# Kernel tuning notes

Hardware: AMD Instinct MI355X
Metric: run time of the kernel (lower is better)

## Reference

```python
import jax, jax.numpy as jnp
import numpy as np

N, E = 10000, 320000
IN, H, C, ED = 256, 4, 64, 64
HC = H * C
EPS = 1e-5
NEG_SLOPE = 0.2


def setup_inputs() -> dict:
    key = jax.random.key(0)
    ks = jax.random.split(key, 12)
    g = lambda k, shape, fan: jax.random.normal(k, shape, jnp.float32) * (1.0 / np.sqrt(fan))
    return {
        "x": jax.random.normal(ks[0], (N, IN), jnp.float32),
        "edge_index": jax.random.randint(ks[1], (2, E), 0, N, jnp.int64),
        "edge_attr": jax.random.normal(ks[2], (E, ED), jnp.float32),
        "Wl": g(ks[3], (HC, IN), IN),   # lin_l weight (source)
        "bl": jnp.zeros((HC,), jnp.float32),
        "Wr": g(ks[4], (HC, IN), IN),   # lin_r weight (target)
        "br": jnp.zeros((HC,), jnp.float32),
        "We": g(ks[5], (HC, ED), ED),   # lin_edge weight (no bias)
        "att": g(ks[6], (H, C), C),
        "bias": jnp.zeros((HC,), jnp.float32),
        "gamma": jnp.ones((HC,), jnp.float32),
        "beta": jnp.zeros((HC,), jnp.float32),
    }


def reference(x, edge_index, edge_attr, Wl, bl, Wr, br, We, att, bias, gamma, beta):
    src, dst = edge_index[0], edge_index[1]
    # add_self_loops with fill_value='mean': loop edge_attr = mean of incoming attrs
    ones = jnp.ones((E,), jnp.float32)
    cnt = jax.ops.segment_sum(ones, dst, num_segments=N)              # [N]
    loop_attr = jax.ops.segment_sum(edge_attr, dst, num_segments=N) / jnp.maximum(cnt, 1.0)[:, None]
    node_ids = jnp.arange(N, dtype=src.dtype)
    src_f = jnp.concatenate([src, node_ids])                          # [E+N]
    dst_f = jnp.concatenate([dst, node_ids])
    ea = jnp.concatenate([edge_attr, loop_attr], axis=0)              # [E+N, ED]

    xl = (x @ Wl.T + bl).reshape(N, H, C)   # source-side projection
    xr = (x @ Wr.T + br).reshape(N, H, C)   # target-side projection
    ep = (ea @ We.T).reshape(-1, H, C)       # edge projection

    m = xl[src_f] + xr[dst_f] + ep                                    # [E+N, H, C]
    m = jnp.where(m >= 0, m, NEG_SLOPE * m)                           # leaky_relu(0.2)
    logits = jnp.einsum("ehc,hc->eh", m, att)                        # [E+N, H]

    # segment softmax over target node dst_f (every node has a self loop)
    mx = jax.ops.segment_max(logits, dst_f, num_segments=N)
    ex = jnp.exp(logits - mx[dst_f])
    den = jax.ops.segment_sum(ex, dst_f, num_segments=N)
    alpha = ex / den[dst_f]                                           # [E+N, H]

    out = jax.ops.segment_sum(xl[src_f] * alpha[:, :, None], dst_f, num_segments=N)
    h = out.reshape(N, HC) + bias

    # SiLU then LayerNorm, dropout is identity in eval
    h = h * jax.nn.sigmoid(h)
    mu = jnp.mean(h, axis=-1, keepdims=True)
    var = jnp.mean((h - mu) ** 2, axis=-1, keepdims=True)
    h = (h - mu) * jax.lax.rsqrt(var + EPS) * gamma + beta
    return h, alpha
```

## Files before the change

kernel.cpp:

```cpp
#include <hip/hip_runtime.h>

#define N_NODES 10000
#define N_EDGES 320000
#define NE_TOT  330000
#define NEG_SLOPE 0.2f
#define LN_EPS 1e-5f

#define OFF_CNT    0u
#define OFF_FILL   40000u
#define OFF_ROWPTR 80128u
#define OFF_EIDS   120320u
#define OFF_POSE   1440512u
#define OFF_XLH    4000512u
#define OFF_XRH    9120512u
#define OFF_LOG    14240512u
#define OFF_WLF    19520512u
#define OFF_WRF    19651584u
#define OFF_WEF    19782656u
#define OFF_SD     19815424u
#define OFF_EAC    21135424u

typedef __bf16 bf16x8 __attribute__((ext_vector_type(8)));
typedef float  f32x4  __attribute__((ext_vector_type(4)));
typedef unsigned short us4 __attribute__((ext_vector_type(4)));

__device__ __forceinline__ float bf2f(unsigned short u) {
    union { unsigned int i; float f; } v;
    v.i = ((unsigned int)u) << 16;
    return v.f;
}
__device__ __forceinline__ float lo2f(unsigned int u) {
    union { unsigned int i; float f; } v;
    v.i = u << 16;
    return v.f;
}
__device__ __forceinline__ float hi2f(unsigned int u) {
    union { unsigned int i; float f; } v;
    v.i = u & 0xFFFF0000u;
    return v.f;
}
__device__ __forceinline__ unsigned short f2bf(float x) {
    __bf16 b = (__bf16)x;
    return __builtin_bit_cast(unsigned short, b);
}
__device__ __forceinline__ bf16x8 cvt8(const float* p) {
    float4 v0 = *reinterpret_cast<const float4*>(p);
    float4 v1 = *reinterpret_cast<const float4*>(p + 4);
    bf16x8 t;
    t[0] = (__bf16)v0.x; t[1] = (__bf16)v0.y; t[2] = (__bf16)v0.z; t[3] = (__bf16)v0.w;
    t[4] = (__bf16)v1.x; t[5] = (__bf16)v1.y; t[6] = (__bf16)v1.z; t[7] = (__bf16)v1.w;
    return t;
}

__global__ void k_count(const int* __restrict__ ei, int* __restrict__ cnt) {
    int e = blockIdx.x * blockDim.x + threadIdx.x;
    if (e < N_EDGES) atomicAdd(&cnt[ei[N_EDGES + e]], 1);
}

__global__ void k_scan(const int* __restrict__ cnt, int* __restrict__ row_ptr) {
    __shared__ int sums[1024];
    int t = threadIdx.x;
    const int CH = 10;
    int base = t * CH;
    int s = 0;
    for (int i = 0; i < CH; i++) {
        int n = base + i;
        if (n < N_NODES) s += cnt[n] + 1;
    }
    sums[t] = s;
    __syncthreads();
    for (int off = 1; off < 1024; off <<= 1) {
        int v = (t >= off) ? sums[t - off] : 0;
        __syncthreads();
        sums[t] += v;
        __syncthreads();
    }
    int run = (t == 0) ? 0 : sums[t - 1];
    for (int i = 0; i < CH; i++) {
        int n = base + i;
        if (n < N_NODES) { row_ptr[n] = run; run += cnt[n] + 1; }
    }
    if (t == 1023) row_ptr[N_NODES] = sums[1023];
}

__global__ void k_fill(const int* __restrict__ ei, const int* __restrict__ row_ptr,
                       int* __restrict__ fill, int* __restrict__ eids,
                       int* __restrict__ sdv, int* __restrict__ pose) {
    int e = blockIdx.x * blockDim.x + threadIdx.x;
    if (e >= NE_TOT) return;
    int s, d;
    if (e < N_EDGES) { s = ei[e]; d = ei[N_EDGES + e]; }
    else             { s = e - N_EDGES; d = s; }
    int pos = atomicAdd(&fill[d], 1);
    int p = row_ptr[d] + pos;
    eids[p] = e;
    sdv[p] = s | (d << 16);
    pose[e] = p;
}

__global__ void k_permute_e(const float* __restrict__ edge_attr,
                            const int* __restrict__ pose,
                            unsigned short* __restrict__ eac) {
    int idx = blockIdx.x * blockDim.x + threadIdx.x;
    if (idx >= N_EDGES * 32) return;
    int e = idx >> 5, cp = idx & 31;
    float2 v = reinterpret_cast<const float2*>(edge_attr)[(size_t)e * 32 + cp];
    int p = pose[e];
    unsigned int u = ((unsigned int)f2bf(v.x)) | (((unsigned int)f2bf(v.y)) << 16);
    reinterpret_cast<unsigned int*>(eac)[(size_t)p * 32 + cp] = u;
}

__global__ void k_self_attr(const int* __restrict__ row_ptr,
                            const int* __restrict__ pose,
                            unsigned short* __restrict__ eac) {
    int node = (blockIdx.x << 2) + (threadIdx.x >> 6);
    int lane = threadIdx.x & 63;
    int b = row_ptr[node], en = row_ptr[node + 1];
    int selfp = pose[N_EDGES + node];
    float s0 = 0.0f, s1 = 0.0f;
    int i = b;
    for (; i + 1 < en; i += 2) {
        float a0 = bf2f(eac[(size_t)(i + 0) * 64 + lane]);
        float a1 = bf2f(eac[(size_t)(i + 1) * 64 + lane]);
        s0 += (i + 0 == selfp) ? 0.0f : a0;
        s1 += (i + 1 == selfp) ? 0.0f : a1;
    }
    for (; i < en; i++) {
        float a = bf2f(eac[(size_t)i * 64 + lane]);
        s0 += (i == selfp) ? 0.0f : a;
    }
    float s = s0 + s1;
    float c = (float)(en - b - 1);
    eac[(size_t)selfp * 64 + lane] = f2bf(s / fmaxf(c, 1.0f));
}

__global__ void k_prep_wfrag(const float* __restrict__ Wl,
                             const float* __restrict__ Wr,
                             const float* __restrict__ We,
                             unsigned short* __restrict__ wlf,
                             unsigned short* __restrict__ wrf,
                             unsigned short* __restrict__ wef) {
    int idx = blockIdx.x * 256 + threadIdx.x;
    if (idx >= 8192) return;
    int ln = idx & 63;
    int ts = (idx >> 6) & 7;
    int ct = idx >> 9;
    int c = ct * 16 + (ln & 15);
    int k0 = ts * 32 + (ln >> 4) * 8;
    *reinterpret_cast<bf16x8*>(wlf + (size_t)idx * 8) = cvt8(Wl + (size_t)c * 256 + k0);
    *reinterpret_cast<bf16x8*>(wrf + (size_t)idx * 8) = cvt8(Wr + (size_t)c * 256 + k0);
    if (idx < 2048) {
        int f = idx >> 6;
        int cb = f >> 1, step = f & 1;
        int ce = cb * 16 + (ln & 15);
        int ke = step * 32 + (ln >> 4) * 8;
        *reinterpret_cast<bf16x8*>(wef + (size_t)idx * 8) = cvt8(We + (size_t)ce * 64 + ke);
    }
}

__global__ __launch_bounds__(256) void k_gemm_mfma(
        const float* __restrict__ x,
        const float* __restrict__ bl, const float* __restrict__ br,
        const unsigned short* __restrict__ wlf,
        const unsigned short* __restrict__ wrf,
        unsigned short* __restrict__ xlh,
        unsigned short* __restrict__ xrh) {
    __shared__ __bf16 xs[8 * 64 * 8];
    int tid = threadIdx.x;
    int nb = blockIdx.x * 16;

    for (int f = tid; f < 512; f += 256) {
        int t = f >> 6, ln = f & 63;
        int node = nb + (ln & 15);
        int k0 = t * 32 + (ln >> 4) * 8;
        *reinterpret_cast<bf16x8*>(&xs[f * 8]) = cvt8(x + (size_t)node * 256 + k0);
    }
    __syncthreads();

    int lane = tid & 63;
    int wv = tid >> 6;
    int quad = lane >> 4;
    int ln15 = lane & 15;

    bf16x8 bfr[8];
#pragma unroll
    for (int t = 0; t < 8; t++)
        bfr[t] = *reinterpret_cast<const bf16x8*>(&xs[(t * 64 + lane) * 8]);

    int node = nb + ln15;
#pragma unroll
    for (int ci = 0; ci < 4; ci++) {
        int ct = wv * 4 + ci;
        f32x4 accl, accr;
        accl[0] = accl[1] = accl[2] = accl[3] = 0.0f;
        accr[0] = accr[1] = accr[2] = accr[3] = 0.0f;
#pragma unroll
        for (int t = 0; t < 8; t++) {
            bf16x8 al = *reinterpret_cast<const bf16x8*>(
                wlf + ((size_t)(ct * 8 + t) * 64 + lane) * 8);
            accl = __builtin_amdgcn_mfma_f32_16x16x32_bf16(al, bfr[t], accl, 0, 0, 0);
        }
#pragma unroll
        for (int t = 0; t < 8; t++) {
            bf16x8 ar = *reinterpret_cast<const bf16x8*>(
                wrf + ((size_t)(ct * 8 + t) * 64 + lane) * 8);
            accr = __builtin_amdgcn_mfma_f32_16x16x32_bf16(ar, bfr[t], accr, 0, 0, 0);
        }
        int cbase = ct * 16 + quad * 4;
        float4 blv = *reinterpret_cast<const float4*>(bl + cbase);
        float4 brv = *reinterpret_cast<const float4*>(br + cbase);
        us4 ol, orr;
        ol[0] = f2bf(accl[0] + blv.x); ol[1] = f2bf(accl[1] + blv.y);
        ol[2] = f2bf(accl[2] + blv.z); ol[3] = f2bf(accl[3] + blv.w);
        orr[0] = f2bf(accr[0] + brv.x); orr[1] = f2bf(accr[1] + brv.y);
        orr[2] = f2bf(accr[2] + brv.z); orr[3] = f2bf(accr[3] + brv.w);
        *reinterpret_cast<us4*>(xlh + (size_t)node * 256 + cbase) = ol;
        *reinterpret_cast<us4*>(xrh + (size_t)node * 256 + cbase) = orr;
    }
}

__global__ __launch_bounds__(256) void k_logits_mfma(
        const int* __restrict__ sdv,
        const unsigned short* __restrict__ eac,
        const unsigned short* __restrict__ xlh,
        const unsigned short* __restrict__ xrh,
        const unsigned short* __restrict__ wef,
        const float* __restrict__ att,
        float* __restrict__ logits) {
    __shared__ __bf16 wef_s[2048 * 8];
    __shared__ float att_s[256];
    int tid = threadIdx.x;

    for (int f = tid; f < 2048; f += 256) {
        *reinterpret_cast<bf16x8*>(&wef_s[(size_t)f * 8]) =
            *reinterpret_cast<const bf16x8*>(wef + (size_t)f * 8);
    }
    if (tid < 64) {
        reinterpret_cast<float4*>(att_s)[tid] =
            reinterpret_cast<const float4*>(att)[tid];
    }
    __syncthreads();

    int lane = tid & 63;
    int wv = tid >> 6;
    int quad = lane >> 4;
    int ln15 = lane & 15;

    const int ntiles = NE_TOT / 16;
#pragma unroll 1
    for (int t = blockIdx.x * 4 + wv; t < ntiles; t += gridDim.x * 4) {
        int pos = t * 16 + ln15;
        int sd = sdv[pos];
        int s = sd & 0xFFFF;
        int d = sd >> 16;
        const unsigned short* row = eac + (size_t)pos * 64;
        const uint2* xls = reinterpret_cast<const uint2*>(xlh + (size_t)s * 256);
        const uint2* xrd = reinterpret_cast<const uint2*>(xrh + (size_t)d * 256);

        bf16x8 bfr0 = *reinterpret_cast<const bf16x8*>(row + quad * 8);
        bf16x8 bfr1 = *reinterpret_cast<const bf16x8*>(row + 32 + quad * 8);
        uint2 xa[16], xb[16];
#pragma unroll
        for (int cb = 0; cb < 16; cb++) {
            int ci = cb * 4 + quad;
            xa[cb] = xls[ci];
            xb[cb] = xrd[ci];
        }
#pragma unroll
        for (int cb = 0; cb < 16; cb++) {
            asm volatile("" : "+v"(xa[cb].x), "+v"(xa[cb].y),
                              "+v"(xb[cb].x), "+v"(xb[cb].y));
        }
        __builtin_amdgcn_sched_barrier(0);

        float hsum[4] = {0.0f, 0.0f, 0.0f, 0.0f};
#pragma unroll
        for (int cb = 0; cb < 16; cb++) {
            f32x4 acc;
            acc[0] = acc[1] = acc[2] = acc[3] = 0.0f;
            bf16x8 a0 = *reinterpret_cast<const bf16x8*>(
                &wef_s[((size_t)(cb * 2 + 0) * 64 + lane) * 8]);
            bf16x8 a1 = *reinterpret_cast<const bf16x8*>(
                &wef_s[((size_t)(cb * 2 + 1) * 64 + lane) * 8]);
            acc = __builtin_amdgcn_mfma_f32_16x16x32_bf16(a0, bfr0, acc, 0, 0, 0);
            acc = __builtin_amdgcn_mfma_f32_16x16x32_bf16(a1, bfr1, acc, 0, 0, 0);

            int cbase = cb * 16 + quad * 4;
            float4 at = *reinterpret_cast<const float4*>(&att_s[cbase]);
            float x0 = lo2f(xa[cb].x) + lo2f(xb[cb].x);
            float x1 = hi2f(xa[cb].x) + hi2f(xb[cb].x);
            float x2 = lo2f(xa[cb].y) + lo2f(xb[cb].y);
            float x3 = hi2f(xa[cb].y) + hi2f(xb[cb].y);
            float v0 = acc[0] + x0; v0 = fmaxf(v0, NEG_SLOPE * v0);
            float v1 = acc[1] + x1; v1 = fmaxf(v1, NEG_SLOPE * v1);
            float v2 = acc[2] + x2; v2 = fmaxf(v2, NEG_SLOPE * v2);
            float v3 = acc[3] + x3; v3 = fmaxf(v3, NEG_SLOPE * v3);
            float hs = fmaf(v0, at.x, fmaf(v1, at.y, fmaf(v2, at.z, v3 * at.w)));
            hsum[cb >> 2] += hs;
        }
#pragma unroll
        for (int hh = 0; hh < 4; hh++) {
            hsum[hh] += __shfl_xor(hsum[hh], 16, 64);
            hsum[hh] += __shfl_xor(hsum[hh], 32, 64);
        }
        if (quad == 0) {
            reinterpret_cast<float4*>(logits)[pos] =
                make_float4(hsum[0], hsum[1], hsum[2], hsum[3]);
        }
    }
}

__global__ void k_aggregate(const int* __restrict__ sdv,
                            const int* __restrict__ row_ptr,
                            const int* __restrict__ eids,
                            const float* __restrict__ logits,
                            const unsigned short* __restrict__ xlh,
                            const float* __restrict__ bias,
                            const float* __restrict__ gamma,
                            const float* __restrict__ beta,
                            float* __restrict__ hout,
                            float* __restrict__ alpha_out) {
    int node = (blockIdx.x << 2) + (threadIdx.x >> 6);
    int lane = threadIdx.x & 63;
    int h = lane >> 4;
    int b = row_ptr[node], en = row_ptr[node + 1];
    const uint2* xl2 = reinterpret_cast<const uint2*>(xlh);

    float m0 = -INFINITY, m1 = -INFINITY, m2 = -INFINITY, m3 = -INFINITY;
    int i = b;
    for (; i + 3 < en; i += 4) {
        m0 = fmaxf(m0, logits[(i + 0) * 4 + h]);
        m1 = fmaxf(m1, logits[(i + 1) * 4 + h]);
        m2 = fmaxf(m2, logits[(i + 2) * 4 + h]);
        m3 = fmaxf(m3, logits[(i + 3) * 4 + h]);
    }
    for (; i < en; i++) m0 = fmaxf(m0, logits[i * 4 + h]);
    float mh = fmaxf(fmaxf(m0, m1), fmaxf(m2, m3));

    float d0 = 0.0f, d1 = 0.0f, d2 = 0.0f, d3 = 0.0f;
    i = b;
    for (; i + 3 < en; i += 4) {
        d0 += __expf(logits[(i + 0) * 4 + h] - mh);
        d1 += __expf(logits[(i + 1) * 4 + h] - mh);
        d2 += __expf(logits[(i + 2) * 4 + h] - mh);
        d3 += __expf(logits[(i + 3) * 4 + h] - mh);
    }
    for (; i < en; i++) d0 += __expf(logits[i * 4 + h] - mh);
    float rden = 1.0f / ((d0 + d1) + (d2 + d3));

    float4 ac0; ac0.x = ac0.y = ac0.z = ac0.w = 0.0f;
    float4 ac1; ac1.x = ac1.y = ac1.z = ac1.w = 0.0f;
    i = b;
    for (; i + 7 < en; i += 8) {
        int sd0 = sdv[i + 0], sd1 = sdv[i + 1], sd2 = sdv[i + 2], sd3 = sdv[i + 3];
        int sd4 = sdv[i + 4], sd5 = sdv[i + 5], sd6 = sdv[i + 6], sd7 = sdv[i + 7];
        float lg0 = logits[(i + 0) * 4 + h], lg1 = logits[(i + 1) * 4 + h];
        float lg2 = logits[(i + 2) * 4 + h], lg3 = logits[(i + 3) * 4 + h];
        float lg4 = logits[(i + 4) * 4 + h], lg5 = logits[(i + 5) * 4 + h];
        float lg6 = logits[(i + 6) * 4 + h], lg7 = logits[(i + 7) * 4 + h];
        int e0 = eids[i + 0], e1 = eids[i + 1], e2 = eids[i + 2], e3 = eids[i + 3];
        int e4 = eids[i + 4], e5 = eids[i + 5], e6 = eids[i + 6], e7 = eids[i + 7];
        uint2 x0 = xl2[(size_t)(sd0 & 0xFFFF) * 64 + lane];
        uint2 x1 = xl2[(size_t)(sd1 & 0xFFFF) * 64 + lane];
        uint2 x2 = xl2[(size_t)(sd2 & 0xFFFF) * 64 + lane];
        uint2 x3 = xl2[(size_t)(sd3 & 0xFFFF) * 64 + lane];
        uint2 x4 = xl2[(size_t)(sd4 & 0xFFFF) * 64 + lane];
        uint2 x5 = xl2[(size_t)(sd5 & 0xFFFF) * 64 + lane];
        uint2 x6 = xl2[(size_t)(sd6 & 0xFFFF) * 64 + lane];
        uint2 x7 = xl2[(size_t)(sd7 & 0xFFFF) * 64 + lane];
        asm volatile("" : "+v"(x0.x), "+v"(x0.y), "+v"(x1.x), "+v"(x1.y),
                          "+v"(x2.x), "+v"(x2.y), "+v"(x3.x), "+v"(x3.y));
        asm volatile("" : "+v"(x4.x), "+v"(x4.y), "+v"(x5.x), "+v"(x5.y),
                          "+v"(x6.x), "+v"(x6.y), "+v"(x7.x), "+v"(x7.y));

        float al0 = __expf(lg0 - mh) * rden;
        float al1 = __expf(lg1 - mh) * rden;
        float al2 = __expf(lg2 - mh) * rden;
        float al3 = __expf(lg3 - mh) * rden;
        float al4 = __expf(lg4 - mh) * rden;
        float al5 = __expf(lg5 - mh) * rden;
        float al6 = __expf(lg6 - mh) * rden;
        float al7 = __expf(lg7 - mh) * rden;
        if ((lane & 15) == 0) {
            alpha_out[e0 * 4 + h] = al0; alpha_out[e1 * 4 + h] = al1;
            alpha_out[e2 * 4 + h] = al2; alpha_out[e3 * 4 + h] = al3;
            alpha_out[e4 * 4 + h] = al4; alpha_out[e5 * 4 + h] = al5;
            alpha_out[e6 * 4 + h] = al6; alpha_out[e7 * 4 + h] = al7;
        }
        ac0.x = fmaf(al0, lo2f(x0.x), ac0.x); ac0.y = fmaf(al0, hi2f(x0.x), ac0.y);
        ac0.z = fmaf(al0, lo2f(x0.y), ac0.z); ac0.w = fmaf(al0, hi2f(x0.y), ac0.w);
        ac1.x = fmaf(al1, lo2f(x1.x), ac1.x); ac1.y = fmaf(al1, hi2f(x1.x), ac1.y);
        ac1.z = fmaf(al1, lo2f(x1.y), ac1.z); ac1.w = fmaf(al1, hi2f(x1.y), ac1.w);
        ac0.x = fmaf(al2, lo2f(x2.x), ac0.x); ac0.y = fmaf(al2, hi2f(x2.x), ac0.y);
        ac0.z = fmaf(al2, lo2f(x2.y), ac0.z); ac0.w = fmaf(al2, hi2f(x2.y), ac0.w);
        ac1.x = fmaf(al3, lo2f(x3.x), ac1.x); ac1.y = fmaf(al3, hi2f(x3.x), ac1.y);
        ac1.z = fmaf(al3, lo2f(x3.y), ac1.z); ac1.w = fmaf(al3, hi2f(x3.y), ac1.w);
        ac0.x = fmaf(al4, lo2f(x4.x), ac0.x); ac0.y = fmaf(al4, hi2f(x4.x), ac0.y);
        ac0.z = fmaf(al4, lo2f(x4.y), ac0.z); ac0.w = fmaf(al4, hi2f(x4.y), ac0.w);
        ac1.x = fmaf(al5, lo2f(x5.x), ac1.x); ac1.y = fmaf(al5, hi2f(x5.x), ac1.y);
        ac1.z = fmaf(al5, lo2f(x5.y), ac1.z); ac1.w = fmaf(al5, hi2f(x5.y), ac1.w);
        ac0.x = fmaf(al6, lo2f(x6.x), ac0.x); ac0.y = fmaf(al6, hi2f(x6.x), ac0.y);
        ac0.z = fmaf(al6, lo2f(x6.y), ac0.z); ac0.w = fmaf(al6, hi2f(x6.y), ac0.w);
        ac1.x = fmaf(al7, lo2f(x7.x), ac1.x); ac1.y = fmaf(al7, hi2f(x7.x), ac1.y);
        ac1.z = fmaf(al7, lo2f(x7.y), ac1.z); ac1.w = fmaf(al7, hi2f(x7.y), ac1.w);
    }
    for (; i < en; i++) {
        int e = eids[i];
        int s = sdv[i] & 0xFFFF;
        float al = __expf(logits[i * 4 + h] - mh) * rden;
        if ((lane & 15) == 0) alpha_out[e * 4 + h] = al;
        uint2 xv = xl2[(size_t)s * 64 + lane];
        ac0.x = fmaf(al, lo2f(xv.x), ac0.x); ac0.y = fmaf(al, hi2f(xv.x), ac0.y);
        ac0.z = fmaf(al, lo2f(xv.y), ac0.z); ac0.w = fmaf(al, hi2f(xv.y), ac0.w);
    }
    float4 acc;
    acc.x = ac0.x + ac1.x;
    acc.y = ac0.y + ac1.y;
    acc.z = ac0.z + ac1.z;
    acc.w = ac0.w + ac1.w;

    const float4 b4 = reinterpret_cast<const float4*>(bias)[lane];
    float4 hv;
    hv.x = acc.x + b4.x; hv.y = acc.y + b4.y;
    hv.z = acc.z + b4.z; hv.w = acc.w + b4.w;
    hv.x = hv.x / (1.0f + __expf(-hv.x));
    hv.y = hv.y / (1.0f + __expf(-hv.y));
    hv.z = hv.z / (1.0f + __expf(-hv.z));
    hv.w = hv.w / (1.0f + __expf(-hv.w));
    float s1 = hv.x + hv.y + hv.z + hv.w;
    float s2 = hv.x * hv.x + hv.y * hv.y + hv.z * hv.z + hv.w * hv.w;
#pragma unroll
    for (int off = 1; off < 64; off <<= 1) {
        s1 += __shfl_xor(s1, off, 64);
        s2 += __shfl_xor(s2, off, 64);
    }
    float mu = s1 * (1.0f / 256.0f);
    float var = s2 * (1.0f / 256.0f) - mu * mu;
    float rs = rsqrtf(var + LN_EPS);
    const float4 g4 = reinterpret_cast<const float4*>(gamma)[lane];
    const float4 be4 = reinterpret_cast<const float4*>(beta)[lane];
    float4 o;
    o.x = (hv.x - mu) * rs * g4.x + be4.x;
    o.y = (hv.y - mu) * rs * g4.y + be4.y;
    o.z = (hv.z - mu) * rs * g4.z + be4.z;
    o.w = (hv.w - mu) * rs * g4.w + be4.w;
    reinterpret_cast<float4*>(hout)[node * 64 + lane] = o;
}

extern "C" void kernel_launch(void* const* d_in, const int* in_sizes, int n_in,
                              void* d_out, int out_size, void* d_ws, size_t ws_size,
                              hipStream_t stream) {
    (void)in_sizes; (void)n_in; (void)out_size; (void)ws_size;
    const float* x         = (const float*)d_in[0];
    const int*   ei        = (const int*)d_in[1];
    const float* edge_attr = (const float*)d_in[2];
    const float* Wl        = (const float*)d_in[3];
    const float* bl        = (const float*)d_in[4];
    const float* Wr        = (const float*)d_in[5];
    const float* br        = (const float*)d_in[6];
    const float* We        = (const float*)d_in[7];
    const float* att       = (const float*)d_in[8];
    const float* bias      = (const float*)d_in[9];
    const float* gamma     = (const float*)d_in[10];
    const float* beta      = (const float*)d_in[11];

    char* ws = (char*)d_ws;
    int*   cnt     = (int*)(ws + OFF_CNT);
    int*   fill    = (int*)(ws + OFF_FILL);
    int*   row_ptr = (int*)(ws + OFF_ROWPTR);
    int*   eids    = (int*)(ws + OFF_EIDS);
    int*   pose    = (int*)(ws + OFF_POSE);
    unsigned short* xlh = (unsigned short*)(ws + OFF_XLH);
    unsigned short* xrh = (unsigned short*)(ws + OFF_XRH);
    float* logits  = (float*)(ws + OFF_LOG);
    unsigned short* wlf = (unsigned short*)(ws + OFF_WLF);
    unsigned short* wrf = (unsigned short*)(ws + OFF_WRF);
    unsigned short* wef = (unsigned short*)(ws + OFF_WEF);
    int*   sdv     = (int*)(ws + OFF_SD);
    unsigned short* eac = (unsigned short*)(ws + OFF_EAC);

    float* hout      = (float*)d_out;
    float* alpha_out = (float*)d_out + N_NODES * 256;

    hipMemsetAsync(ws + OFF_CNT, 0, 2 * N_NODES * sizeof(int), stream);

    k_count<<<(N_EDGES + 255) / 256, 256, 0, stream>>>(ei, cnt);
    k_scan<<<1, 1024, 0, stream>>>(cnt, row_ptr);
    k_prep_wfrag<<<32, 256, 0, stream>>>(Wl, Wr, We, wlf, wrf, wef);
    k_fill<<<(NE_TOT + 255) / 256, 256, 0, stream>>>(ei, row_ptr, fill, eids, sdv, pose);
    k_gemm_mfma<<<N_NODES / 16, 256, 0, stream>>>(x, bl, br, wlf, wrf, xlh, xrh);
    k_permute_e<<<(N_EDGES * 32) / 256, 256, 0, stream>>>(edge_attr, pose, eac);
    k_self_attr<<<N_NODES / 4, 256, 0, stream>>>(row_ptr, pose, eac);
    k_logits_mfma<<<2048, 256, 0, stream>>>(sdv, eac, xlh, xrh, wef, att, logits);
    k_aggregate<<<N_NODES / 4, 256, 0, stream>>>(sdv, row_ptr, eids, logits, xlh,
                                                 bias, gamma, beta, hout, alpha_out);
}
```

Baseline: 354.1 us.

## Restructure logits kernel to stage edge projections in LDS and gather rows coalesced

```diff
diff --git a/kernel.cpp b/kernel.cpp
--- a/kernel.cpp
+++ b/kernel.cpp
@@ -219,93 +219,75 @@
     }
 }
 
-__global__ __launch_bounds__(256) void k_logits_mfma(
+__global__ __launch_bounds__(256) void k_logits_v2(
         const int* __restrict__ sdv,
         const unsigned short* __restrict__ eac,
+        const unsigned short* __restrict__ wef,
         const unsigned short* __restrict__ xlh,
         const unsigned short* __restrict__ xrh,
-        const unsigned short* __restrict__ wef,
         const float* __restrict__ att,
         float* __restrict__ logits) {
-    __shared__ __bf16 wef_s[2048 * 8];
-    __shared__ float att_s[256];
+    __shared__ unsigned short ep_s[4][4096];
     int tid = threadIdx.x;
-
-    for (int f = tid; f < 2048; f += 256) {
-        *reinterpret_cast<bf16x8*>(&wef_s[(size_t)f * 8]) =
-            *reinterpret_cast<const bf16x8*>(wef + (size_t)f * 8);
-    }
-    if (tid < 64) {
-        reinterpret_cast<float4*>(att_s)[tid] =
-            reinterpret_cast<const float4*>(att)[tid];
-    }
-    __syncthreads();
-
-    int lane = tid & 63;
-    int wv = tid >> 6;
-    int quad = lane >> 4;
-    int ln15 = lane & 15;
+    int wv = tid >> 6, lane = tid & 63;
+    int h = lane >> 4, l15 = lane & 15;
+    unsigned short* eps = ep_s[wv];
+
+    const uint2* xl2 = reinterpret_cast<const uint2*>(xlh);
+    const uint2* xr2 = reinterpret_cast<const uint2*>(xrh);
+    float4 atv = reinterpret_cast<const float4*>(att)[lane];
+
+    int wswz = (l15 & 3) << 4;
 
     const int ntiles = NE_TOT / 16;
 #pragma unroll 1
     for (int t = blockIdx.x * 4 + wv; t < ntiles; t += gridDim.x * 4) {
-        int pos = t * 16 + ln15;
-        int sd = sdv[pos];
-        int s = sd & 0xFFFF;
-        int d = sd >> 16;
-        const unsigned short* row = eac + (size_t)pos * 64;
-        const uint2* xls = reinterpret_cast<const uint2*>(xlh + (size_t)s * 256);
-        const uint2* xrd = reinterpret_cast<const uint2*>(xrh + (size_t)d * 256);
-
-        bf16x8 bfr0 = *reinterpret_cast<const bf16x8*>(row + quad * 8);
-        bf16x8 bfr1 = *reinterpret_cast<const bf16x8*>(row + 32 + quad * 8);
-        uint2 xa[16], xb[16];
-#pragma unroll
-        for (int cb = 0; cb < 16; cb++) {
-            int ci = cb * 4 + quad;
-            xa[cb] = xls[ci];
-            xb[cb] = xrd[ci];
-        }
-#pragma unroll
-        for (int cb = 0; cb < 16; cb++) {
-            asm volatile("" : "+v"(xa[cb].x), "+v"(xa[cb].y),
-                              "+v"(xb[cb].x), "+v"(xb[cb].y));
-        }
-        __builtin_amdgcn_sched_barrier(0);
-
-        float hsum[4] = {0.0f, 0.0f, 0.0f, 0.0f};
+        int pos0 = t * 16;
+        int sdl = sdv[pos0 + l15];
+
+        const unsigned short* row = eac + (size_t)(pos0 + l15) * 64;
+        bf16x8 b0 = *reinterpret_cast<const bf16x8*>(row + h * 8);
+        bf16x8 b1 = *reinterpret_cast<const bf16x8*>(row + 32 + h * 8);
 #pragma unroll
         for (int cb = 0; cb < 16; cb++) {
             f32x4 acc;
             acc[0] = acc[1] = acc[2] = acc[3] = 0.0f;
             bf16x8 a0 = *reinterpret_cast<const bf16x8*>(
-                &wef_s[((size_t)(cb * 2 + 0) * 64 + lane) * 8]);
+                wef + ((size_t)(cb * 2 + 0) * 64 + lane) * 8);
             bf16x8 a1 = *reinterpret_cast<const bf16x8*>(
-                &wef_s[((size_t)(cb * 2 + 1) * 64 + lane) * 8]);
-            acc = __builtin_amdgcn_mfma_f32_16x16x32_bf16(a0, bfr0, acc, 0, 0, 0);
-            acc = __builtin_amdgcn_mfma_f32_16x16x32_bf16(a1, bfr1, acc, 0, 0, 0);
-
-            int cbase = cb * 16 + quad * 4;
-            float4 at = *reinterpret_cast<const float4*>(&att_s[cbase]);
-            float x0 = lo2f(xa[cb].x) + lo2f(xb[cb].x);
-            float x1 = hi2f(xa[cb].x) + hi2f(xb[cb].x);
-            float x2 = lo2f(xa[cb].y) + lo2f(xb[cb].y);
-            float x3 = hi2f(xa[cb].y) + hi2f(xb[cb].y);
-            float v0 = acc[0] + x0; v0 = fmaxf(v0, NEG_SLOPE * v0);
-            float v1 = acc[1] + x1; v1 = fmaxf(v1, NEG_SLOPE * v1);
-            float v2 = acc[2] + x2; v2 = fmaxf(v2, NEG_SLOPE * v2);
-            float v3 = acc[3] + x3; v3 = fmaxf(v3, NEG_SLOPE * v3);
-            float hs = fmaf(v0, at.x, fmaf(v1, at.y, fmaf(v2, at.z, v3 * at.w)));
-            hsum[cb >> 2] += hs;
+                wef + ((size_t)(cb * 2 + 1) * 64 + lane) * 8);
+            acc = __builtin_amdgcn_mfma_f32_16x16x32_bf16(a0, b0, acc, 0, 0, 0);
+            acc = __builtin_amdgcn_mfma_f32_16x16x32_bf16(a1, b1, acc, 0, 0, 0);
+            us4 o;
+            o[0] = f2bf(acc[0]); o[1] = f2bf(acc[1]);
+            o[2] = f2bf(acc[2]); o[3] = f2bf(acc[3]);
+            *reinterpret_cast<us4*>(&eps[l15 * 256 + ((cb * 16 + h * 4) ^ wswz)]) = o;
         }
-#pragma unroll
-        for (int hh = 0; hh < 4; hh++) {
-            hsum[hh] += __shfl_xor(hsum[hh], 16, 64);
-            hsum[hh] += __shfl_xor(hsum[hh], 32, 64);
-        }
-        if (quad == 0) {
-            reinterpret_cast<float4*>(logits)[pos] =
-                make_float4(hsum[0], hsum[1], hsum[2], hsum[3]);
+
+#pragma unroll 4
+        for (int j = 0; j < 16; j++) {
+            int pos = pos0 + j;
+            int sd = __shfl(sdl, j, 64);
+            int s = sd & 0xFFFF;
+            int d = sd >> 16;
+            uint2 xlv = xl2[(size_t)s * 64 + lane];
+            uint2 xrv = xr2[(size_t)d * 64 + lane];
+            us4 epv = *reinterpret_cast<const us4*>(
+                &eps[j * 256 + ((lane * 4) ^ ((j & 3) << 4))]);
+            float v0 = lo2f(xlv.x) + lo2f(xrv.x) + bf2f(epv[0]);
+            v0 = fmaxf(v0, NEG_SLOPE * v0);
+            float v1 = hi2f(xlv.x) + hi2f(xrv.x) + bf2f(epv[1]);
+            v1 = fmaxf(v1, NEG_SLOPE * v1);
+            float v2 = lo2f(xlv.y) + lo2f(xrv.y) + bf2f(epv[2]);
+            v2 = fmaxf(v2, NEG_SLOPE * v2);
+            float v3 = hi2f(xlv.y) + hi2f(xrv.y) + bf2f(epv[3]);
+            v3 = fmaxf(v3, NEG_SLOPE * v3);
+            float hs = fmaf(v0, atv.x, fmaf(v1, atv.y, fmaf(v2, atv.z, v3 * atv.w)));
+            hs += __shfl_xor(hs, 1, 64);
+            hs += __shfl_xor(hs, 2, 64);
+            hs += __shfl_xor(hs, 4, 64);
+            hs += __shfl_xor(hs, 8, 64);
+            if (l15 == 0) logits[(size_t)pos * 4 + h] = hs;
         }
     }
 }
@@ -351,41 +333,22 @@
     float4 ac0; ac0.x = ac0.y = ac0.z = ac0.w = 0.0f;
     float4 ac1; ac1.x = ac1.y = ac1.z = ac1.w = 0.0f;
     i = b;
-    for (; i + 7 < en; i += 8) {
+    for (; i + 3 < en; i += 4) {
         int sd0 = sdv[i + 0], sd1 = sdv[i + 1], sd2 = sdv[i + 2], sd3 = sdv[i + 3];
-        int sd4 = sdv[i + 4], sd5 = sdv[i + 5], sd6 = sdv[i + 6], sd7 = sdv[i + 7];
         float lg0 = logits[(i + 0) * 4 + h], lg1 = logits[(i + 1) * 4 + h];
         float lg2 = logits[(i + 2) * 4 + h], lg3 = logits[(i + 3) * 4 + h];
-        float lg4 = logits[(i + 4) * 4 + h], lg5 = logits[(i + 5) * 4 + h];
-        float lg6 = logits[(i + 6) * 4 + h], lg7 = logits[(i + 7) * 4 + h];
         int e0 = eids[i + 0], e1 = eids[i + 1], e2 = eids[i + 2], e3 = eids[i + 3];
-        int e4 = eids[i + 4], e5 = eids[i + 5], e6 = eids[i + 6], e7 = eids[i + 7];
         uint2 x0 = xl2[(size_t)(sd0 & 0xFFFF) * 64 + lane];
         uint2 x1 = xl2[(size_t)(sd1 & 0xFFFF) * 64 + lane];
         uint2 x2 = xl2[(size_t)(sd2 & 0xFFFF) * 64 + lane];
         uint2 x3 = xl2[(size_t)(sd3 & 0xFFFF) * 64 + lane];
-        uint2 x4 = xl2[(size_t)(sd4 & 0xFFFF) * 64 + lane];
-        uint2 x5 = xl2[(size_t)(sd5 & 0xFFFF) * 64 + lane];
-        uint2 x6 = xl2[(size_t)(sd6 & 0xFFFF) * 64 + lane];
-        uint2 x7 = xl2[(size_t)(sd7 & 0xFFFF) * 64 + lane];
-        asm volatile("" : "+v"(x0.x), "+v"(x0.y), "+v"(x1.x), "+v"(x1.y),
-                          "+v"(x2.x), "+v"(x2.y), "+v"(x3.x), "+v"(x3.y));
-        asm volatile("" : "+v"(x4.x), "+v"(x4.y), "+v"(x5.x), "+v"(x5.y),
-                          "+v"(x6.x), "+v"(x6.y), "+v"(x7.x), "+v"(x7.y));
-
         float al0 = __expf(lg0 - mh) * rden;
         float al1 = __expf(lg1 - mh) * rden;
         float al2 = __expf(lg2 - mh) * rden;
         float al3 = __expf(lg3 - mh) * rden;
-        float al4 = __expf(lg4 - mh) * rden;
-        float al5 = __expf(lg5 - mh) * rden;
-        float al6 = __expf(lg6 - mh) * rden;
-        float al7 = __expf(lg7 - mh) * rden;
         if ((lane & 15) == 0) {
             alpha_out[e0 * 4 + h] = al0; alpha_out[e1 * 4 + h] = al1;
             alpha_out[e2 * 4 + h] = al2; alpha_out[e3 * 4 + h] = al3;
-            alpha_out[e4 * 4 + h] = al4; alpha_out[e5 * 4 + h] = al5;
-            alpha_out[e6 * 4 + h] = al6; alpha_out[e7 * 4 + h] = al7;
         }
         ac0.x = fmaf(al0, lo2f(x0.x), ac0.x); ac0.y = fmaf(al0, hi2f(x0.x), ac0.y);
         ac0.z = fmaf(al0, lo2f(x0.y), ac0.z); ac0.w = fmaf(al0, hi2f(x0.y), ac0.w);
@@ -395,14 +358,6 @@
         ac0.z = fmaf(al2, lo2f(x2.y), ac0.z); ac0.w = fmaf(al2, hi2f(x2.y), ac0.w);
         ac1.x = fmaf(al3, lo2f(x3.x), ac1.x); ac1.y = fmaf(al3, hi2f(x3.x), ac1.y);
         ac1.z = fmaf(al3, lo2f(x3.y), ac1.z); ac1.w = fmaf(al3, hi2f(x3.y), ac1.w);
-        ac0.x = fmaf(al4, lo2f(x4.x), ac0.x); ac0.y = fmaf(al4, hi2f(x4.x), ac0.y);
-        ac0.z = fmaf(al4, lo2f(x4.y), ac0.z); ac0.w = fmaf(al4, hi2f(x4.y), ac0.w);
-        ac1.x = fmaf(al5, lo2f(x5.x), ac1.x); ac1.y = fmaf(al5, hi2f(x5.x), ac1.y);
-        ac1.z = fmaf(al5, lo2f(x5.y), ac1.z); ac1.w = fmaf(al5, hi2f(x5.y), ac1.w);
-        ac0.x = fmaf(al6, lo2f(x6.x), ac0.x); ac0.y = fmaf(al6, hi2f(x6.x), ac0.y);
-        ac0.z = fmaf(al6, lo2f(x6.y), ac0.z); ac0.w = fmaf(al6, hi2f(x6.y), ac0.w);
-        ac1.x = fmaf(al7, lo2f(x7.x), ac1.x); ac1.y = fmaf(al7, hi2f(x7.x), ac1.y);
-        ac1.z = fmaf(al7, lo2f(x7.y), ac1.z); ac1.w = fmaf(al7, hi2f(x7.y), ac1.w);
     }
     for (; i < en; i++) {
         int e = eids[i];
@@ -491,7 +446,7 @@
     k_gemm_mfma<<<N_NODES / 16, 256, 0, stream>>>(x, bl, br, wlf, wrf, xlh, xrh);
     k_permute_e<<<(N_EDGES * 32) / 256, 256, 0, stream>>>(edge_attr, pose, eac);
     k_self_attr<<<N_NODES / 4, 256, 0, stream>>>(row_ptr, pose, eac);
-    k_logits_mfma<<<2048, 256, 0, stream>>>(sdv, eac, xlh, xrh, wef, att, logits);
+    k_logits_v2<<<1024, 256, 0, stream>>>(sdv, eac, wef, xlh, xrh, att, logits);
     k_aggregate<<<N_NODES / 4, 256, 0, stream>>>(sdv, row_ptr, eids, logits, xlh,
                                                  bias, gamma, beta, hout, alpha_out);
 }
```

Result: slower. 400.8 us (+13.2%).

## Permute xl/xr feature layout for 16-byte gathers and fuse count with weight prep

Applied to the files above, without the earlier changes.

```diff
diff --git a/kernel.cpp b/kernel.cpp
--- a/kernel.cpp
+++ b/kernel.cpp
@@ -20,6 +20,7 @@
 #define OFF_SD     19815424u
 #define OFF_EAC    21135424u
 
+
 typedef __bf16 bf16x8 __attribute__((ext_vector_type(8)));
 typedef float  f32x4  __attribute__((ext_vector_type(4)));
 typedef unsigned short us4 __attribute__((ext_vector_type(4)));
@@ -52,9 +53,33 @@
     return t;
 }
 
-__global__ void k_count(const int* __restrict__ ei, int* __restrict__ cnt) {
-    int e = blockIdx.x * blockDim.x + threadIdx.x;
-    if (e < N_EDGES) atomicAdd(&cnt[ei[N_EDGES + e]], 1);
+__global__ void k_pre(const int* __restrict__ ei, int* __restrict__ cnt,
+                      const float* __restrict__ Wl, const float* __restrict__ Wr,
+                      const float* __restrict__ We,
+                      unsigned short* __restrict__ wlf,
+                      unsigned short* __restrict__ wrf,
+                      unsigned short* __restrict__ wef) {
+    int gid = blockIdx.x * 256 + threadIdx.x;
+    if (gid < 8192) {
+        int idx = gid;
+        int ln = idx & 63;
+        int ts = (idx >> 6) & 7;
+        int ct = idx >> 9;
+        int c = ct * 16 + (ln & 15);
+        int k0 = ts * 32 + (ln >> 4) * 8;
+        *reinterpret_cast<bf16x8*>(wlf + (size_t)idx * 8) = cvt8(Wl + (size_t)c * 256 + k0);
+        *reinterpret_cast<bf16x8*>(wrf + (size_t)idx * 8) = cvt8(Wr + (size_t)c * 256 + k0);
+        if (idx < 2048) {
+            int f = idx >> 6;
+            int cb = f >> 1, step = f & 1;
+            int ce = cb * 16 + (ln & 15);
+            int ke = step * 32 + (ln >> 4) * 8;
+            *reinterpret_cast<bf16x8*>(wef + (size_t)idx * 8) = cvt8(We + (size_t)ce * 64 + ke);
+        }
+    } else {
+        int e = gid - 8192;
+        if (e < N_EDGES) atomicAdd(&cnt[ei[N_EDGES + e]], 1);
+    }
 }
 
 __global__ void k_scan(const int* __restrict__ cnt, int* __restrict__ row_ptr) {
@@ -134,30 +159,6 @@
     eac[(size_t)selfp * 64 + lane] = f2bf(s / fmaxf(c, 1.0f));
 }
 
-__global__ void k_prep_wfrag(const float* __restrict__ Wl,
-                             const float* __restrict__ Wr,
-                             const float* __restrict__ We,
-                             unsigned short* __restrict__ wlf,
-                             unsigned short* __restrict__ wrf,
-                             unsigned short* __restrict__ wef) {
-    int idx = blockIdx.x * 256 + threadIdx.x;
-    if (idx >= 8192) return;
-    int ln = idx & 63;
-    int ts = (idx >> 6) & 7;
-    int ct = idx >> 9;
-    int c = ct * 16 + (ln & 15);
-    int k0 = ts * 32 + (ln >> 4) * 8;
-    *reinterpret_cast<bf16x8*>(wlf + (size_t)idx * 8) = cvt8(Wl + (size_t)c * 256 + k0);
-    *reinterpret_cast<bf16x8*>(wrf + (size_t)idx * 8) = cvt8(Wr + (size_t)c * 256 + k0);
-    if (idx < 2048) {
-        int f = idx >> 6;
-        int cb = f >> 1, step = f & 1;
-        int ce = cb * 16 + (ln & 15);
-        int ke = step * 32 + (ln >> 4) * 8;
-        *reinterpret_cast<bf16x8*>(wef + (size_t)idx * 8) = cvt8(We + (size_t)ce * 64 + ke);
-    }
-}
-
 __global__ __launch_bounds__(256) void k_gemm_mfma(
         const float* __restrict__ x,
         const float* __restrict__ bl, const float* __restrict__ br,
@@ -207,6 +208,7 @@
             accr = __builtin_amdgcn_mfma_f32_16x16x32_bf16(ar, bfr[t], accr, 0, 0, 0);
         }
         int cbase = ct * 16 + quad * 4;
+        int fidx  = quad * 64 + ct * 4;
         float4 blv = *reinterpret_cast<const float4*>(bl + cbase);
         float4 brv = *reinterpret_cast<const float4*>(br + cbase);
         us4 ol, orr;
@@ -214,12 +216,12 @@
         ol[2] = f2bf(accl[2] + blv.z); ol[3] = f2bf(accl[3] + blv.w);
         orr[0] = f2bf(accr[0] + brv.x); orr[1] = f2bf(accr[1] + brv.y);
         orr[2] = f2bf(accr[2] + brv.z); orr[3] = f2bf(accr[3] + brv.w);
-        *reinterpret_cast<us4*>(xlh + (size_t)node * 256 + cbase) = ol;
-        *reinterpret_cast<us4*>(xrh + (size_t)node * 256 + cbase) = orr;
-    }
-}
-
-__global__ __launch_bounds__(256) void k_logits_mfma(
+        *reinterpret_cast<us4*>(xlh + (size_t)node * 256 + fidx) = ol;
+        *reinterpret_cast<us4*>(xrh + (size_t)node * 256 + fidx) = orr;
+    }
+}
+
+__global__ __launch_bounds__(256) void k_logits_v4(
         const int* __restrict__ sdv,
         const unsigned short* __restrict__ eac,
         const unsigned short* __restrict__ xlh,
@@ -254,22 +256,18 @@
         int s = sd & 0xFFFF;
         int d = sd >> 16;
         const unsigned short* row = eac + (size_t)pos * 64;
-        const uint2* xls = reinterpret_cast<const uint2*>(xlh + (size_t)s * 256);
-        const uint2* xrd = reinterpret_cast<const uint2*>(xrh + (size_t)d * 256);
+        const uint4* xls = reinterpret_cast<const uint4*>(
+            xlh + (size_t)s * 256 + quad * 64);
+        const uint4* xrd = reinterpret_cast<const uint4*>(
+            xrh + (size_t)d * 256 + quad * 64);
 
         bf16x8 bfr0 = *reinterpret_cast<const bf16x8*>(row + quad * 8);
         bf16x8 bfr1 = *reinterpret_cast<const bf16x8*>(row + 32 + quad * 8);
-        uint2 xa[16], xb[16];
-#pragma unroll
-        for (int cb = 0; cb < 16; cb++) {
-            int ci = cb * 4 + quad;
-            xa[cb] = xls[ci];
-            xb[cb] = xrd[ci];
-        }
-#pragma unroll
-        for (int cb = 0; cb < 16; cb++) {
-            asm volatile("" : "+v"(xa[cb].x), "+v"(xa[cb].y),
-                              "+v"(xb[cb].x), "+v"(xb[cb].y));
+        uint4 xa[8], xb[8];
+#pragma unroll
+        for (int k = 0; k < 8; k++) {
+            xa[k] = xls[k];
+            xb[k] = xrd[k];
         }
         __builtin_amdgcn_sched_barrier(0);
 
@@ -285,16 +283,17 @@
             acc = __builtin_amdgcn_mfma_f32_16x16x32_bf16(a0, bfr0, acc, 0, 0, 0);
             acc = __builtin_amdgcn_mfma_f32_16x16x32_bf16(a1, bfr1, acc, 0, 0, 0);
 
+            unsigned int u0 = (cb & 1) ? xa[cb >> 1].z : xa[cb >> 1].x;
+            unsigned int u1 = (cb & 1) ? xa[cb >> 1].w : xa[cb >> 1].y;
+            unsigned int w0 = (cb & 1) ? xb[cb >> 1].z : xb[cb >> 1].x;
+            unsigned int w1 = (cb & 1) ? xb[cb >> 1].w : xb[cb >> 1].y;
+
             int cbase = cb * 16 + quad * 4;
             float4 at = *reinterpret_cast<const float4*>(&att_s[cbase]);
-            float x0 = lo2f(xa[cb].x) + lo2f(xb[cb].x);
-            float x1 = hi2f(xa[cb].x) + hi2f(xb[cb].x);
-            float x2 = lo2f(xa[cb].y) + lo2f(xb[cb].y);
-            float x3 = hi2f(xa[cb].y) + hi2f(xb[cb].y);
-            float v0 = acc[0] + x0; v0 = fmaxf(v0, NEG_SLOPE * v0);
-            float v1 = acc[1] + x1; v1 = fmaxf(v1, NEG_SLOPE * v1);
-            float v2 = acc[2] + x2; v2 = fmaxf(v2, NEG_SLOPE * v2);
-            float v3 = acc[3] + x3; v3 = fmaxf(v3, NEG_SLOPE * v3);
+            float v0 = acc[0] + lo2f(u0) + lo2f(w0); v0 = fmaxf(v0, NEG_SLOPE * v0);
+            float v1 = acc[1] + hi2f(u0) + hi2f(w0); v1 = fmaxf(v1, NEG_SLOPE * v1);
+            float v2 = acc[2] + lo2f(u1) + lo2f(w1); v2 = fmaxf(v2, NEG_SLOPE * v2);
+            float v3 = acc[3] + hi2f(u1) + hi2f(w1); v3 = fmaxf(v3, NEG_SLOPE * v3);
             float hs = fmaf(v0, at.x, fmaf(v1, at.y, fmaf(v2, at.z, v3 * at.w)));
             hsum[cb >> 2] += hs;
         }
@@ -325,6 +324,8 @@
     int h = lane >> 4;
     int b = row_ptr[node], en = row_ptr[node + 1];
     const uint2* xl2 = reinterpret_cast<const uint2*>(xlh);
+    int ci  = (lane & 3) * 16 + (lane >> 2);
+    int cb4 = (lane >> 2) * 4 + (lane & 3);
 
     float m0 = -INFINITY, m1 = -INFINITY, m2 = -INFINITY, m3 = -INFINITY;
     int i = b;
@@ -360,14 +361,14 @@
         float lg6 = logits[(i + 6) * 4 + h], lg7 = logits[(i + 7) * 4 + h];
         int e0 = eids[i + 0], e1 = eids[i + 1], e2 = eids[i + 2], e3 = eids[i + 3];
         int e4 = eids[i + 4], e5 = eids[i + 5], e6 = eids[i + 6], e7 = eids[i + 7];
-        uint2 x0 = xl2[(size_t)(sd0 & 0xFFFF) * 64 + lane];
-        uint2 x1 = xl2[(size_t)(sd1 & 0xFFFF) * 64 + lane];
-        uint2 x2 = xl2[(size_t)(sd2 & 0xFFFF) * 64 + lane];
-        uint2 x3 = xl2[(size_t)(sd3 & 0xFFFF) * 64 + lane];
-        uint2 x4 = xl2[(size_t)(sd4 & 0xFFFF) * 64 + lane];
-        uint2 x5 = xl2[(size_t)(sd5 & 0xFFFF) * 64 + lane];
-        uint2 x6 = xl2[(size_t)(sd6 & 0xFFFF) * 64 + lane];
-        uint2 x7 = xl2[(size_t)(sd7 & 0xFFFF) * 64 + lane];
+        uint2 x0 = xl2[(size_t)(sd0 & 0xFFFF) * 64 + ci];
+        uint2 x1 = xl2[(size_t)(sd1 & 0xFFFF) * 64 + ci];
+        uint2 x2 = xl2[(size_t)(sd2 & 0xFFFF) * 64 + ci];
+        uint2 x3 = xl2[(size_t)(sd3 & 0xFFFF) * 64 + ci];
+        uint2 x4 = xl2[(size_t)(sd4 & 0xFFFF) * 64 + ci];
+        uint2 x5 = xl2[(size_t)(sd5 & 0xFFFF) * 64 + ci];
+        uint2 x6 = xl2[(size_t)(sd6 & 0xFFFF) * 64 + ci];
+        uint2 x7 = xl2[(size_t)(sd7 & 0xFFFF) * 64 + ci];
         asm volatile("" : "+v"(x0.x), "+v"(x0.y), "+v"(x1.x), "+v"(x1.y),
                           "+v"(x2.x), "+v"(x2.y), "+v"(x3.x), "+v"(x3.y));
         asm volatile("" : "+v"(x4.x), "+v"(x4.y), "+v"(x5.x), "+v"(x5.y),
@@ -409,7 +410,7 @@
         int s = sdv[i] & 0xFFFF;
         float al = __expf(logits[i * 4 + h] - mh) * rden;
         if ((lane & 15) == 0) alpha_out[e * 4 + h] = al;
-        uint2 xv = xl2[(size_t)s * 64 + lane];
+        uint2 xv = xl2[(size_t)s * 64 + ci];
         ac0.x = fmaf(al, lo2f(xv.x), ac0.x); ac0.y = fmaf(al, hi2f(xv.x), ac0.y);
         ac0.z = fmaf(al, lo2f(xv.y), ac0.z); ac0.w = fmaf(al, hi2f(xv.y), ac0.w);
     }
@@ -419,7 +420,7 @@
     acc.z = ac0.z + ac1.z;
     acc.w = ac0.w + ac1.w;
 
-    const float4 b4 = reinterpret_cast<const float4*>(bias)[lane];
+    const float4 b4 = reinterpret_cast<const float4*>(bias)[cb4];
     float4 hv;
     hv.x = acc.x + b4.x; hv.y = acc.y + b4.y;
     hv.z = acc.z + b4.z; hv.w = acc.w + b4.w;
@@ -437,14 +438,14 @@
     float mu = s1 * (1.0f / 256.0f);
     float var = s2 * (1.0f / 256.0f) - mu * mu;
     float rs = rsqrtf(var + LN_EPS);
-    const float4 g4 = reinterpret_cast<const float4*>(gamma)[lane];
-    const float4 be4 = reinterpret_cast<const float4*>(beta)[lane];
+    const float4 g4 = reinterpret_cast<const float4*>(gamma)[cb4];
+    const float4 be4 = reinterpret_cast<const float4*>(beta)[cb4];
     float4 o;
     o.x = (hv.x - mu) * rs * g4.x + be4.x;
     o.y = (hv.y - mu) * rs * g4.y + be4.y;
     o.z = (hv.z - mu) * rs * g4.z + be4.z;
     o.w = (hv.w - mu) * rs * g4.w + be4.w;
-    reinterpret_cast<float4*>(hout)[node * 64 + lane] = o;
+    reinterpret_cast<float4*>(hout)[node * 64 + cb4] = o;
 }
 
 extern "C" void kernel_launch(void* const* d_in, const int* in_sizes, int n_in,
@@ -484,14 +485,14 @@
 
     hipMemsetAsync(ws + OFF_CNT, 0, 2 * N_NODES * sizeof(int), stream);
 
-    k_count<<<(N_EDGES + 255) / 256, 256, 0, stream>>>(ei, cnt);
+    k_pre<<<(8192 + N_EDGES) / 256, 256, 0, stream>>>(ei, cnt, Wl, Wr, We,
+                                                      wlf, wrf, wef);
     k_scan<<<1, 1024, 0, stream>>>(cnt, row_ptr);
-    k_prep_wfrag<<<32, 256, 0, stream>>>(Wl, Wr, We, wlf, wrf, wef);
     k_fill<<<(NE_TOT + 255) / 256, 256, 0, stream>>>(ei, row_ptr, fill, eids, sdv, pose);
     k_gemm_mfma<<<N_NODES / 16, 256, 0, stream>>>(x, bl, br, wlf, wrf, xlh, xrh);
     k_permute_e<<<(N_EDGES * 32) / 256, 256, 0, stream>>>(edge_attr, pose, eac);
     k_self_attr<<<N_NODES / 4, 256, 0, stream>>>(row_ptr, pose, eac);
-    k_logits_mfma<<<2048, 256, 0, stream>>>(sdv, eac, xlh, xrh, wef, att, logits);
+    k_logits_v4<<<2048, 256, 0, stream>>>(sdv, eac, xlh, xrh, wef, att, logits);
     k_aggregate<<<N_NODES / 4, 256, 0, stream>>>(sdv, row_ptr, eids, logits, xlh,
                                                  bias, gamma, beta, hout, alpha_out);
 }
```

Result: no change. 358.2 us (+1.2%).
